# Kernel tuning notes

Hardware: AMD Instinct MI355X
Metric: run time of the kernel (lower is better)

The kernel has to match this reference:

```python
import jax, jax.numpy as jnp
import numpy as np

N_SUBJECTS = 64
N_LABELS = 16
DENS_TEMP = 0.1  # args.ProtoSim_dens_temp


def setup_inputs() -> dict:
    key = jax.random.key(0)
    k1, k2, k3 = jax.random.split(key, 3)
    B, V, D = 16384, 2, 512
    X_data = jax.random.normal(k1, (B, V, D), dtype=jnp.float32)
    subject = jax.random.randint(k2, (B,), 0, N_SUBJECTS)
    labels = jax.random.randint(k3, (B,), 0, N_LABELS)
    return {"X_data": X_data, "subject": subject, "labels": labels}


def reference(X_data, subject, labels):
    B, V, D = X_data.shape  # V == contrast_count == 2 (code doubles subject/labels once)
    K = N_SUBJECTS * N_LABELS
    # torch.cat(torch.unbind(X, dim=1), dim=0) -> [V*B, D]
    cf = jnp.transpose(X_data, (1, 0, 2)).reshape(V * B, D)
    subj2 = jnp.concatenate([subject, subject])
    lab2 = jnp.concatenate([labels, labels])
    # group id: groups enumerated sorted-by-(subject,label), i.e. g = s*C + l
    gid = subj2 * N_LABELS + lab2
    ones = jnp.ones((V * B,), dtype=cf.dtype)
    counts = jax.ops.segment_sum(ones, gid, num_segments=K)  # [K]
    safe_cnt = jnp.maximum(counts, 1.0)
    centroid = jax.ops.segment_sum(cf, gid, num_segments=K) / safe_cnt[:, None]  # [K, D]
    # per-sample euclidean distance to own group centroid (torch.cdist)
    dist = jnp.linalg.norm(cf - centroid[gid], axis=1)  # [V*B]
    # density_g = mean(sqrt(dist)) / log(n_g + 10) for n_g > 1, else dmax; then clip & scale
    mean_sqrt = jax.ops.segment_sum(jnp.sqrt(dist), gid, num_segments=K) / safe_cnt
    density = mean_sqrt / jnp.log(counts + 10.0)
    density = jnp.where(counts > 1, density, 0.0)
    density = jnp.where(counts > 1, density, density.max())
    density = jnp.clip(density, jnp.percentile(density, 10), jnp.percentile(density, 90))
    density = DENS_TEMP * density / density.mean()
    density = jax.lax.stop_gradient(density)  # torch builds it via .tolist()/numpy
    # mask: different subject AND same label vs each group prototype
    g_subj = jnp.arange(K) // N_LABELS
    g_lab = jnp.arange(K) % N_LABELS
    mask = ((subj2[:, None] != g_subj[None, :]) & (lab2[:, None] == g_lab[None, :])).astype(cf.dtype)  # [V*B, K]
    # with N_SUBJECTS > 1 every row has >= 1 positive group -> no rows deleted
    sim = jnp.matmul(cf, centroid.T) / density[None, :]  # [V*B, K]
    sim = sim - jax.lax.stop_gradient(jnp.max(sim, axis=1, keepdims=True))
    positive_sim = sim * mask
    # CrossEntropyLoss(reduction='none') with soft (unnormalized) targets = mask
    logp = jax.nn.log_softmax(positive_sim, axis=1)
    loss_per_row = -(mask * logp).sum(axis=1) / mask.sum(axis=1)
    return loss_per_row.mean()
```

## Files before the change

### kernel.cpp

```cpp
#include <hip/hip_runtime.h>


typedef __bf16 v8bf __attribute__((ext_vector_type(8)));
typedef __bf16 v4bf __attribute__((ext_vector_type(4)));
typedef float  v4f  __attribute__((ext_vector_type(4)));
typedef unsigned int u32x4 __attribute__((ext_vector_type(4)));

#define B_ROWS 16384
#define ROWS   32768
#define NGRP   1024
#define DIM    512
#define LOG2E  1.4426950408889634f
#define LN2    0.6931471805599453f

__device__ __forceinline__ float wredSum(float v){
#pragma unroll
  for (int o = 32; o > 0; o >>= 1) v += __shfl_xor(v, o);
  return v;
}
__device__ __forceinline__ float wredMax(float v){
#pragma unroll
  for (int o = 32; o > 0; o >>= 1) v = fmaxf(v, __shfl_xor(v, o));
  return v;
}

__global__ void kA2(const int* __restrict__ subj, const int* __restrict__ lab,
                    int* __restrict__ base_cnt, int* __restrict__ gid_arr){
  int i = blockIdx.x * 256 + threadIdx.x;
  int g = subj[i] * 16 + lab[i];
  gid_arr[i] = g;
  atomicAdd(&base_cnt[g], 1);
}

__global__ void kA3(const int* __restrict__ base_cnt, int* __restrict__ offs,
                    int* __restrict__ fillp){
  __shared__ int sb[NGRP];
  int t = threadIdx.x;
  int c = base_cnt[t];
  sb[t] = c;
  __syncthreads();
  for (int off = 1; off < NGRP; off <<= 1){
    int v = (t >= off) ? sb[t - off] : 0;
    __syncthreads();
    sb[t] += v;
    __syncthreads();
  }
  int ex = sb[t] - c;
  offs[t] = ex;
  fillp[t] = ex;
}

__global__ void kA4(const int* __restrict__ gid_arr, int* __restrict__ fillp,
                    int* __restrict__ row_list){
  int i = blockIdx.x * 256 + threadIdx.x;
  int pos = atomicAdd(&fillp[gid_arr[i]], 1);
  row_list[pos] = i;
}

__global__ void kB(const float* __restrict__ X, const int* __restrict__ base_cnt,
                   const int* __restrict__ offs, const int* __restrict__ row_list,
                   float* __restrict__ cent_f, __bf16* __restrict__ cent_b){
  int g = blockIdx.x, t = threadIdx.x;
  int n = base_cnt[g], off = offs[g];
  float ax = 0.f, ay = 0.f, az = 0.f, aw = 0.f;
  for (int j = 0; j < n; ++j){
    int r = row_list[off + j];
    const float4* p = (const float4*)(X + (size_t)r * 1024);
    float4 a = p[t];
    float4 b = p[t + 128];
    ax += a.x + b.x; ay += a.y + b.y; az += a.z + b.z; aw += a.w + b.w;
  }
  int cnt2 = 2 * n;
  float inv = 1.0f / (float)(cnt2 > 1 ? cnt2 : 1);
  float4 c; c.x = ax * inv; c.y = ay * inv; c.z = az * inv; c.w = aw * inv;
  ((float4*)(cent_f + (size_t)g * DIM))[t] = c;
  v4bf cb; cb[0] = (__bf16)c.x; cb[1] = (__bf16)c.y; cb[2] = (__bf16)c.z; cb[3] = (__bf16)c.w;
  *(v4bf*)(cent_b + (size_t)g * DIM + t * 4) = cb;
}

__global__ void kC(const float* __restrict__ X, const int* __restrict__ subj,
                   const int* __restrict__ lab, const float* __restrict__ cent_f,
                   float* __restrict__ msq, __bf16* __restrict__ cfb){
  int w = threadIdx.x >> 6, lane = threadIdx.x & 63;
  int r = blockIdx.x * 4 + w;
  int i = r & (B_ROWS - 1), v = r >> 14;
  int g = subj[i] * 16 + lab[i];
  const float4* xr = (const float4*)(X + ((size_t)(i * 2 + v)) * DIM);
  const float4* cr = (const float4*)(cent_f + (size_t)g * DIM);
  float4 x0 = xr[lane], x1 = xr[lane + 64];
  float4 c0 = cr[lane], c1 = cr[lane + 64];
  float s = 0.f, d;
  d = x0.x - c0.x; s += d * d;  d = x0.y - c0.y; s += d * d;
  d = x0.z - c0.z; s += d * d;  d = x0.w - c0.w; s += d * d;
  d = x1.x - c1.x; s += d * d;  d = x1.y - c1.y; s += d * d;
  d = x1.z - c1.z; s += d * d;  d = x1.w - c1.w; s += d * d;
  v4bf b0; b0[0]=(__bf16)x0.x; b0[1]=(__bf16)x0.y; b0[2]=(__bf16)x0.z; b0[3]=(__bf16)x0.w;
  v4bf b1; b1[0]=(__bf16)x1.x; b1[1]=(__bf16)x1.y; b1[2]=(__bf16)x1.z; b1[3]=(__bf16)x1.w;
  *(v4bf*)(cfb + (size_t)r * DIM + lane * 4)       = b0;
  *(v4bf*)(cfb + (size_t)r * DIM + 256 + lane * 4) = b1;
  s = wredSum(s);
  if (lane == 0){
    float dist = sqrtf(s);
    atomicAdd(&msq[g], sqrtf(dist));
  }
}

__global__ void kD(const int* __restrict__ base_cnt, const float* __restrict__ msq,
                   float* __restrict__ scale2){
  __shared__ float sd[NGRP];
  __shared__ float ss[NGRP];
  __shared__ float rb[16];
  int t = threadIdx.x;
  int lane = t & 63, wid = t >> 6;
  int cnt2 = 2 * base_cnt[t];
  float safe = (float)(cnt2 > 1 ? cnt2 : 1);
  float v = (msq[t] / safe) / logf((float)cnt2 + 10.0f);
  float d1 = (cnt2 > 1) ? v : 0.0f;
  float wm = wredMax(d1);
  if (lane == 0) rb[wid] = wm;
  __syncthreads();
  float x = (lane < 16) ? rb[lane] : -3.0e38f;
  if (wid == 0){ x = wredMax(x); if (lane == 0) rb[0] = x; }
  __syncthreads();
  float dmax = rb[0];
  float d2 = (cnt2 > 1) ? d1 : dmax;
  sd[t] = d2;
  __syncthreads();
  int rank = 0;
  for (int j = 0; j < NGRP; ++j){
    float dj = sd[j];
    rank += (dj < d2) || (dj == d2 && j < t);
  }
  ss[rank] = d2;
  __syncthreads();
  float p10 = ss[102] + 0.3f * (ss[103] - ss[102]);
  float p90 = ss[920] + 0.7f * (ss[921] - ss[920]);
  float c = fminf(fmaxf(d2, p10), p90);
  __syncthreads();
  float wsm = wredSum(c);
  if (lane == 0) rb[wid] = wsm;
  __syncthreads();
  float y = (lane < 16) ? rb[lane] : 0.0f;
  if (wid == 0){ y = wredSum(y); if (lane == 0) rb[0] = y; }
  __syncthreads();
  float mean = rb[0] * (1.0f / 1024.0f);
  scale2[t] = LOG2E * mean / (0.1f * c);
}

__global__ __launch_bounds__(256)
void kE(const __bf16* __restrict__ cfb, const __bf16* __restrict__ centb,
        const float* __restrict__ scale2, const int* __restrict__ gid_arr,
        float* __restrict__ pm, float* __restrict__ pe, float* __restrict__ ps){
  __shared__ u32x4 smA[1024];
  __shared__ u32x4 smB[1024];
  int tid = threadIdx.x, lane = tid & 63, w = tid >> 6;
  int wr = w >> 1, wc = w & 1;
  int l15 = lane & 15, lhi = lane >> 4;
  int bid = blockIdx.x;
  int nb = bid & 7, mb = bid >> 3;

  const u32x4* gA = (const u32x4*)cfb;
  const u32x4* gB = (const u32x4*)centb;

  int srow = tid >> 1, shalf = tid & 1;
  int swz = srow & 7;
  int arow = (mb * 128 + srow) * 64;
  int brow = (nb * 128 + srow) * 64;
  int lbase = srow * 8;

  v4f acc[4][4];
#pragma unroll
  for (int a1 = 0; a1 < 4; ++a1)
#pragma unroll
    for (int a2 = 0; a2 < 4; ++a2)
      acc[a1][a2] = (v4f){0.f, 0.f, 0.f, 0.f};

  u32x4 av[4], bv[4];
  auto stage_load = [&](int ksv){
    int kb = ksv * 8;
#pragma unroll
    for (int j = 0; j < 4; ++j){
      int idx16 = shalf * 4 + j;
      av[j] = gA[arow + kb + idx16];
      bv[j] = gB[brow + kb + idx16];
    }
  };

  stage_load(0);
  for (int ks = 0; ks < 8; ++ks){
    __syncthreads();
#pragma unroll
    for (int j = 0; j < 4; ++j){
      int idx16 = shalf * 4 + j;
      smA[lbase + (idx16 ^ swz)] = av[j];
      smB[lbase + (idx16 ^ swz)] = bv[j];
    }
    __syncthreads();
    if (ks < 7) stage_load(ks + 1);
#pragma unroll
    for (int kk = 0; kk < 2; ++kk){
      v8bf a[4], b[4];
#pragma unroll
      for (int f = 0; f < 4; ++f){
        int rA = wr * 64 + f * 16 + l15;
        a[f] = __builtin_bit_cast(v8bf, smA[rA * 8 + ((kk * 4 + lhi) ^ (rA & 7))]);
        int rB = wc * 64 + f * 16 + l15;
        b[f] = __builtin_bit_cast(v8bf, smB[rB * 8 + ((kk * 4 + lhi) ^ (rB & 7))]);
      }
#pragma unroll
      for (int fm = 0; fm < 4; ++fm)
#pragma unroll
        for (int fn = 0; fn < 4; ++fn)
          acc[fm][fn] = __builtin_amdgcn_mfma_f32_16x16x32_bf16(a[fm], b[fn], acc[fm][fn], 0, 0, 0);
    }
  }

  int colbase = nb * 128 + wc * 64;
  float sc[4];
#pragma unroll
  for (int fn = 0; fn < 4; ++fn) sc[fn] = scale2[colbase + fn * 16 + l15];
  int gsb = colbase >> 4;
  int slot = nb * 2 + wc;

#pragma unroll
  for (int fm = 0; fm < 4; ++fm){
    int rbase = mb * 128 + wr * 64 + fm * 16 + lhi * 4;
#pragma unroll
    for (int j = 0; j < 4; ++j){
      int row = rbase + j;
      int gr = gid_arr[row & (B_ROWS - 1)];
      float labeq = ((gr & 15) == l15) ? 1.0f : 0.0f;
      int rsub = gr >> 4;
      float vv[4];
      float m2 = -3.0e38f;
#pragma unroll
      for (int fn = 0; fn < 4; ++fn){
        vv[fn] = acc[fm][fn][j] * sc[fn];
        m2 = fmaxf(m2, vv[fn]);
      }
      float e = 0.f, s = 0.f;
#pragma unroll
      for (int fn = 0; fn < 4; ++fn){
        float mk = (rsub != (gsb + fn)) ? labeq : 0.0f;
        e += mk * exp2f(vv[fn] - m2);
        s += mk * vv[fn];
      }
#pragma unroll
      for (int off = 1; off < 16; off <<= 1){
        float mo = __shfl_xor(m2, off);
        float eo = __shfl_xor(e, off);
        float so = __shfl_xor(s, off);
        float mn = fmaxf(m2, mo);
        e = e * exp2f(m2 - mn) + eo * exp2f(mo - mn);
        s += so;
        m2 = mn;
      }
      if (l15 == 0){
        pm[slot * ROWS + row] = m2;
        pe[slot * ROWS + row] = e;
        ps[slot * ROWS + row] = s;
      }
    }
  }
}

__global__ void kF(const float* __restrict__ pm, const float* __restrict__ pe,
                   const float* __restrict__ ps, float* __restrict__ loss_sum){
  int r = blockIdx.x * 256 + threadIdx.x;
  float M = -3.0e38f, E = 0.f, S = 0.f;
#pragma unroll
  for (int p = 0; p < 16; ++p){
    float m = pm[p * ROWS + r];
    float e = pe[p * ROWS + r];
    float s = ps[p * ROWS + r];
    float mn = fmaxf(M, m);
    E = E * exp2f(M - mn) + e * exp2f(m - mn);
    S += s;
    M = mn;
  }
  float loss = logf(961.0f + E) + LN2 * M - LN2 * (S * (1.0f / 63.0f));
  __shared__ float sb[4];
  float wsum = wredSum(loss);
  int lane = threadIdx.x & 63, wid = threadIdx.x >> 6;
  if (lane == 0) sb[wid] = wsum;
  __syncthreads();
  if (threadIdx.x == 0) atomicAdd(loss_sum, sb[0] + sb[1] + sb[2] + sb[3]);
}

__global__ void kG(const float* __restrict__ loss_sum, float* __restrict__ out){
  out[0] = loss_sum[0] * (1.0f / (float)ROWS);
}

extern "C" void kernel_launch(void* const* d_in, const int* in_sizes, int n_in,
                              void* d_out, int out_size, void* d_ws, size_t ws_size,
                              hipStream_t stream){
  const float* X   = (const float*)d_in[0];
  const int* subj  = (const int*)d_in[1];
  const int* lab   = (const int*)d_in[2];
  float* out = (float*)d_out;
  char* ws = (char*)d_ws;

  int*    base_cnt = (int*)(ws + 0);
  float*  msq      = (float*)(ws + 4096);
  float*  loss_s   = (float*)(ws + 8192);
  int*    offs     = (int*)(ws + 8448);
  int*    fillp    = (int*)(ws + 12544);
  int*    gid_arr  = (int*)(ws + 16640);
  int*    row_list = (int*)(ws + 82176);
  float*  scale2   = (float*)(ws + 147712);
  float*  cent_f   = (float*)(ws + 151808);
  __bf16* cent_b   = (__bf16*)(ws + 2248960);
  __bf16* cfb      = (__bf16*)(ws + 3297536);
  float*  pm       = (float*)(ws + 36851968);
  float*  pe       = (float*)(ws + 38949120);
  float*  ps       = (float*)(ws + 41046272);

  hipMemsetAsync(ws, 0, 8208, stream);

  kA2<<<64, 256, 0, stream>>>(subj, lab, base_cnt, gid_arr);
  kA3<<<1, 1024, 0, stream>>>(base_cnt, offs, fillp);
  kA4<<<64, 256, 0, stream>>>(gid_arr, fillp, row_list);
  kB <<<1024, 128, 0, stream>>>(X, base_cnt, offs, row_list, cent_f, cent_b);
  kC <<<8192, 256, 0, stream>>>(X, subj, lab, cent_f, msq, cfb);
  kD <<<1, 1024, 0, stream>>>(base_cnt, msq, scale2);
  kE <<<2048, 256, 0, stream>>>(cfb, cent_b, scale2, gid_arr, pm, pe, ps);
  kF <<<128, 256, 0, stream>>>(pm, pe, ps, loss_s);
  kG <<<1, 1, 0, stream>>>(loss_s, out);
}
```

Before: 183.8 us.

## Fuse similarity GEMM with online softmax loss, keeping rows in registers

The GEMM kernel is restructured so each block owns 64 sample rows held in registers across the full K dimension and streams all 1024 centroids through double-buffered padded shared memory. An online max/exp/sum reduction runs per 128-group tile, so the per-slot partial max/exp/sum arrays and the separate combine kernel are removed. This saves global writes and reads of partials and one launch. In exchange the grid has fewer blocks, register pressure is higher, and the load is split as each of the four wave sub-lanes covering a row contributes a quarter of that row's loss.

```diff
diff --git a/kernel.cpp b/kernel.cpp
--- a/kernel.cpp
+++ b/kernel.cpp
@@ -147,144 +147,134 @@
   scale2[t] = LOG2E * mean / (0.1f * c);
 }
 
-__global__ __launch_bounds__(256)
+__global__ __launch_bounds__(256, 2)
 void kE(const __bf16* __restrict__ cfb, const __bf16* __restrict__ centb,
         const float* __restrict__ scale2, const int* __restrict__ gid_arr,
-        float* __restrict__ pm, float* __restrict__ pe, float* __restrict__ ps){
-  __shared__ u32x4 smA[1024];
-  __shared__ u32x4 smB[1024];
+        float* __restrict__ loss_sum){
+  __shared__ u32x4 cent[2][128 * 9];
+  __shared__ float sscale[NGRP];
+  __shared__ float red[4];
   int tid = threadIdx.x, lane = tid & 63, w = tid >> 6;
-  int wr = w >> 1, wc = w & 1;
   int l15 = lane & 15, lhi = lane >> 4;
-  int bid = blockIdx.x;
-  int nb = bid & 7, mb = bid >> 3;
-
-  const u32x4* gA = (const u32x4*)cfb;
-  const u32x4* gB = (const u32x4*)centb;
-
-  int srow = tid >> 1, shalf = tid & 1;
-  int swz = srow & 7;
-  int arow = (mb * 128 + srow) * 64;
-  int brow = (nb * 128 + srow) * 64;
-  int lbase = srow * 8;
-
-  v4f acc[4][4];
-#pragma unroll
-  for (int a1 = 0; a1 < 4; ++a1)
-#pragma unroll
-    for (int a2 = 0; a2 < 4; ++a2)
-      acc[a1][a2] = (v4f){0.f, 0.f, 0.f, 0.f};
-
-  u32x4 av[4], bv[4];
-  auto stage_load = [&](int ksv){
-    int kb = ksv * 8;
-#pragma unroll
-    for (int j = 0; j < 4; ++j){
-      int idx16 = shalf * 4 + j;
-      av[j] = gA[arow + kb + idx16];
-      bv[j] = gB[brow + kb + idx16];
+  int row = blockIdx.x * 64 + w * 16 + l15;
+
+  const u32x4* gA = (const u32x4*)centb;
+  const u32x4* gB = (const u32x4*)cfb;
+
+  ((v4f*)sscale)[tid] = ((const v4f*)scale2)[tid];
+
+  u32x4 breg[16];
+  {
+    const u32x4* rp = gB + (size_t)row * 64 + lhi;
+#pragma unroll
+    for (int c = 0; c < 16; ++c) breg[c] = rp[c * 4];
+  }
+
+  int g = gid_arr[row & (B_ROWS - 1)];
+  int rsub = g >> 4, rlab = g & 15;
+  float labeq[4];
+#pragma unroll
+  for (int j = 0; j < 4; ++j) labeq[j] = (rlab == lhi * 4 + j) ? 1.0f : 0.0f;
+
+  u32x4 st[4];
+  auto stage = [&](int tt){
+    int gb = tt >> 3, ks = tt & 7;
+#pragma unroll
+    for (int c2 = 0; c2 < 4; ++c2){
+      int flat = c2 * 256 + tid;
+      int mrow = flat >> 3, kidx = flat & 7;
+      st[c2] = gA[(size_t)(gb * 128 + mrow) * 64 + ks * 8 + kidx];
     }
   };
-
-  stage_load(0);
-  for (int ks = 0; ks < 8; ++ks){
-    __syncthreads();
-#pragma unroll
-    for (int j = 0; j < 4; ++j){
-      int idx16 = shalf * 4 + j;
-      smA[lbase + (idx16 ^ swz)] = av[j];
-      smB[lbase + (idx16 ^ swz)] = bv[j];
+  auto commit = [&](int buf){
+#pragma unroll
+    for (int c2 = 0; c2 < 4; ++c2){
+      int flat = c2 * 256 + tid;
+      int mrow = flat >> 3, kidx = flat & 7;
+      cent[buf][mrow * 9 + kidx] = st[c2];
     }
-    __syncthreads();
-    if (ks < 7) stage_load(ks + 1);
-#pragma unroll
-    for (int kk = 0; kk < 2; ++kk){
-      v8bf a[4], b[4];
-#pragma unroll
-      for (int f = 0; f < 4; ++f){
-        int rA = wr * 64 + f * 16 + l15;
-        a[f] = __builtin_bit_cast(v8bf, smA[rA * 8 + ((kk * 4 + lhi) ^ (rA & 7))]);
-        int rB = wc * 64 + f * 16 + l15;
-        b[f] = __builtin_bit_cast(v8bf, smB[rB * 8 + ((kk * 4 + lhi) ^ (rB & 7))]);
+  };
+
+  v4f acc[8];
+#pragma unroll
+  for (int fm = 0; fm < 8; ++fm) acc[fm] = (v4f){0.f, 0.f, 0.f, 0.f};
+  float M = -3.0e38f, E = 0.f, S = 0.f;
+
+  stage(0); commit(0);
+  __syncthreads();
+
+  for (int gb = 0; gb < 8; ++gb){
+#pragma unroll
+    for (int ks = 0; ks < 8; ++ks){
+      int tt = gb * 8 + ks;
+      if (tt < 63) stage(tt + 1);
+#pragma unroll
+      for (int kk = 0; kk < 2; ++kk){
+        v8bf afr[8];
+#pragma unroll
+        for (int fm = 0; fm < 8; ++fm){
+          int mrow = fm * 16 + l15;
+          afr[fm] = __builtin_bit_cast(v8bf, cent[ks & 1][mrow * 9 + kk * 4 + lhi]);
+        }
+#pragma unroll
+        for (int fm = 0; fm < 8; ++fm)
+          acc[fm] = __builtin_amdgcn_mfma_f32_16x16x32_bf16(
+              afr[fm], __builtin_bit_cast(v8bf, breg[ks * 2 + kk]), acc[fm], 0, 0, 0);
       }
-#pragma unroll
-      for (int fm = 0; fm < 4; ++fm)
-#pragma unroll
-        for (int fn = 0; fn < 4; ++fn)
-          acc[fm][fn] = __builtin_amdgcn_mfma_f32_16x16x32_bf16(a[fm], b[fn], acc[fm][fn], 0, 0, 0);
-    }
-  }
-
-  int colbase = nb * 128 + wc * 64;
-  float sc[4];
-#pragma unroll
-  for (int fn = 0; fn < 4; ++fn) sc[fn] = scale2[colbase + fn * 16 + l15];
-  int gsb = colbase >> 4;
-  int slot = nb * 2 + wc;
-
-#pragma unroll
-  for (int fm = 0; fm < 4; ++fm){
-    int rbase = mb * 128 + wr * 64 + fm * 16 + lhi * 4;
-#pragma unroll
-    for (int j = 0; j < 4; ++j){
-      int row = rbase + j;
-      int gr = gid_arr[row & (B_ROWS - 1)];
-      float labeq = ((gr & 15) == l15) ? 1.0f : 0.0f;
-      int rsub = gr >> 4;
-      float vv[4];
-      float m2 = -3.0e38f;
-#pragma unroll
-      for (int fn = 0; fn < 4; ++fn){
-        vv[fn] = acc[fm][fn][j] * sc[fn];
-        m2 = fmaxf(m2, vv[fn]);
-      }
-      float e = 0.f, s = 0.f;
-#pragma unroll
-      for (int fn = 0; fn < 4; ++fn){
-        float mk = (rsub != (gsb + fn)) ? labeq : 0.0f;
-        e += mk * exp2f(vv[fn] - m2);
-        s += mk * vv[fn];
-      }
-#pragma unroll
-      for (int off = 1; off < 16; off <<= 1){
-        float mo = __shfl_xor(m2, off);
-        float eo = __shfl_xor(e, off);
-        float so = __shfl_xor(s, off);
-        float mn = fmaxf(m2, mo);
-        e = e * exp2f(m2 - mn) + eo * exp2f(mo - mn);
-        s += so;
-        m2 = mn;
-      }
-      if (l15 == 0){
-        pm[slot * ROWS + row] = m2;
-        pe[slot * ROWS + row] = e;
-        ps[slot * ROWS + row] = s;
+      if (tt < 63){
+        commit((tt + 1) & 1);
+        __syncthreads();
       }
     }
-  }
-}
-
-__global__ void kF(const float* __restrict__ pm, const float* __restrict__ pe,
-                   const float* __restrict__ ps, float* __restrict__ loss_sum){
-  int r = blockIdx.x * 256 + threadIdx.x;
-  float M = -3.0e38f, E = 0.f, S = 0.f;
-#pragma unroll
-  for (int p = 0; p < 16; ++p){
-    float m = pm[p * ROWS + r];
-    float e = pe[p * ROWS + r];
-    float s = ps[p * ROWS + r];
-    float mn = fmaxf(M, m);
-    E = E * exp2f(M - mn) + e * exp2f(m - mn);
-    S += s;
+    {
+      v4f vs[8];
+      float mloc = -3.0e38f;
+#pragma unroll
+      for (int fm = 0; fm < 8; ++fm){
+        v4f sc = *(const v4f*)&sscale[gb * 128 + fm * 16 + lhi * 4];
+        v4f t;
+#pragma unroll
+        for (int j = 0; j < 4; ++j){
+          t[j] = acc[fm][j] * sc[j];
+          mloc = fmaxf(mloc, t[j]);
+        }
+        vs[fm] = t;
+      }
+      float Mn = fmaxf(M, mloc);
+      float eadd = 0.f, sadd = 0.f;
+#pragma unroll
+      for (int fm = 0; fm < 8; ++fm){
+        float subne = (rsub != gb * 8 + fm) ? 1.0f : 0.0f;
+#pragma unroll
+        for (int j = 0; j < 4; ++j){
+          float mk = subne * labeq[j];
+          eadd += mk * exp2f(vs[fm][j] - Mn);
+          sadd += mk * vs[fm][j];
+        }
+      }
+      E = E * exp2f(M - Mn) + eadd;
+      S += sadd;
+      M = Mn;
+#pragma unroll
+      for (int fm = 0; fm < 8; ++fm) acc[fm] = (v4f){0.f, 0.f, 0.f, 0.f};
+    }
+  }
+
+#pragma unroll
+  for (int off = 16; off < 64; off <<= 1){
+    float mo = __shfl_xor(M, off);
+    float eo = __shfl_xor(E, off);
+    float so = __shfl_xor(S, off);
+    float mn = fmaxf(M, mo);
+    E = E * exp2f(M - mn) + eo * exp2f(mo - mn);
+    S += so;
     M = mn;
   }
   float loss = logf(961.0f + E) + LN2 * M - LN2 * (S * (1.0f / 63.0f));
-  __shared__ float sb[4];
-  float wsum = wredSum(loss);
-  int lane = threadIdx.x & 63, wid = threadIdx.x >> 6;
-  if (lane == 0) sb[wid] = wsum;
-  __syncthreads();
-  if (threadIdx.x == 0) atomicAdd(loss_sum, sb[0] + sb[1] + sb[2] + sb[3]);
+  float wsum = wredSum(loss) * 0.25f;
+  if (lane == 0) red[w] = wsum;
+  __syncthreads();
+  if (tid == 0) atomicAdd(loss_sum, red[0] + red[1] + red[2] + red[3]);
 }
 
 __global__ void kG(const float* __restrict__ loss_sum, float* __restrict__ out){
@@ -311,9 +301,6 @@
   float*  cent_f   = (float*)(ws + 151808);
   __bf16* cent_b   = (__bf16*)(ws + 2248960);
   __bf16* cfb      = (__bf16*)(ws + 3297536);
-  float*  pm       = (float*)(ws + 36851968);
-  float*  pe       = (float*)(ws + 38949120);
-  float*  ps       = (float*)(ws + 41046272);
 
   hipMemsetAsync(ws, 0, 8208, stream);
 
@@ -323,7 +310,6 @@
   kB <<<1024, 128, 0, stream>>>(X, base_cnt, offs, row_list, cent_f, cent_b);
   kC <<<8192, 256, 0, stream>>>(X, subj, lab, cent_f, msq, cfb);
   kD <<<1, 1024, 0, stream>>>(base_cnt, msq, scale2);
-  kE <<<2048, 256, 0, stream>>>(cfb, cent_b, scale2, gid_arr, pm, pe, ps);
-  kF <<<128, 256, 0, stream>>>(pm, pe, ps, loss_s);
+  kE <<<512, 256, 0, stream>>>(cfb, cent_b, scale2, gid_arr, loss_s);
   kG <<<1, 1, 0, stream>>>(loss_s, out);
 }
```

New measurement: 166.8 us. -9.2%, faster.
